# Optimization experiments

Measured on AMD Instinct MI355X. Metric: run time of the kernel, lower is better.

## Reference

```python
import jax, jax.numpy as jnp
import numpy as np

B, C, L, NLAB, EMB, NFREQ, D = 256, 64, 512, 10, 256, 9, 8
FIN, FH, FOUT = 4 * C, C, C
P_TOTAL = FIN * FH + FH + FH * FOUT + FOUT + FIN * FOUT + FOUT


def _leaky(x):
    return jax.nn.leaky_relu(x, 0.2)


def _conv1d(x, w, b=None, pad=0):
    y = jax.lax.conv_general_dilated(x, w, (1,), [(pad, pad)], dimension_numbers=('NCH', 'OIH', 'NCH'))
    return y if b is None else y + b[None, :, None]


def _res1d(x, w0, b0, w1, b1, ws=None, pad=1):
    # GAN-stability style residual block: out = shortcut(x) + 0.1 * conv1(act(conv0(act(x))))
    xs = _conv1d(x, ws) if ws is not None else x
    dx = _conv1d(_leaky(x), w0, b0, pad)
    dx = _conv1d(_leaky(dx), w1, b1, pad)
    return xs + 0.1 * dx


def _pos_enc():
    # sinusoidal positional encoding, 2*NFREQ channels over L positions
    p = np.arange(L, dtype=np.float32)
    f = (np.pi / 2.0 ** np.arange(NFREQ, dtype=np.float32))[:, None]
    pe = np.concatenate([np.sin(f * p), np.cos(f * p)], axis=0)  # [2*NFREQ, L]
    return jnp.asarray(pe)


def _sobel_kernels():
    s = np.array([1.0, 2.0, 1.0], np.float32)
    d = np.array([-1.0, 0.0, 1.0], np.float32)
    kx = np.einsum('i,j,k->ijk', d, s, s)
    ky = np.einsum('i,j,k->ijk', s, d, s)
    kz = np.einsum('i,j,k->ijk', s, s, d)
    return jnp.asarray(np.stack([kx, ky, kz]))  # [3, 3, 3, 3]


def _sin_sobel(x, k):
    # depthwise 3D sobel along each axis, sin of gradients, concat with input -> 4C channels
    outs = [x]
    for i in range(3):
        w = jnp.broadcast_to(k[i][None, None], (C, 1, 3, 3, 3))
        g = jax.lax.conv_general_dilated(x, w, (1, 1, 1), [(1, 1)] * 3,
                                         dimension_numbers=('NCDHW', 'OIDHW', 'NCDHW'),
                                         feature_group_count=C)
        outs.append(jnp.sin(g))
    return jnp.concatenate(outs, axis=1)


def _inst_norm(x):
    m = x.mean(axis=(2, 3, 4), keepdims=True)
    v = x.var(axis=(2, 3, 4), keepdims=True)
    return (x - m) * jax.lax.rsqrt(v + 1e-5)


def _dyna(x, p):
    # hypernet-generated per-sample 1x1x1 residual conv block
    b = x.shape[0]
    xf = x.reshape(b, FIN, D * D * D)
    o = FIN * FH
    wh = p[:, :o].reshape(b, FH, FIN)
    bh = p[:, o:o + FH]; o += FH
    wl = p[:, o:o + FH * FOUT].reshape(b, FOUT, FH); o += FH * FOUT
    bl = p[:, o:o + FOUT]; o += FOUT
    ws = p[:, o:o + FIN * FOUT].reshape(b, FOUT, FIN); o += FIN * FOUT
    bs = p[:, o:o + FOUT]
    xs = jnp.einsum('boi,bis->bos', ws, xf) + bs[:, :, None]
    dx = _leaky(jnp.einsum('bhi,bis->bhs', wh, xf) + bh[:, :, None])
    dx = jnp.einsum('boh,bhs->bos', wl, dx) + bl[:, :, None]
    return (xs + 0.1 * dx).reshape(b, FOUT, D, D, D)


def _forward(codes, y, fc_w, fc_b, in_w0, in_b0, in_w1, in_b1, in_ws, leak, hyper_w, hyper_b,
             out_w0, out_b0, out_w1, out_b1, l1_w0, l1_b0, l1_w1, l1_b1,
             l2_w0, l2_b0, l2_w1, l2_b1, l2_ws):
    b = codes.shape[0]
    yemb = jax.nn.one_hot(y, NLAB, dtype=codes.dtype) @ fc_w.T + fc_b
    yemb = yemb / jnp.maximum(jnp.linalg.norm(yemb, axis=1, keepdims=True), 1e-12)
    pe = jnp.broadcast_to(_pos_enc()[None], (b, 2 * NFREQ, L))
    x = jnp.concatenate([codes, pe], axis=1)  # [B, C+2*NFREQ, L]
    x = _res1d(x, in_w0, in_b0, in_w1, in_b1, ws=in_ws)
    x = x.reshape(b, C, D, D, D)
    leak_c = jnp.clip(leak, 0.001, 1000.0)
    p = yemb @ hyper_w.T + hyper_b  # per-sample dynamic conv params [B, P_TOTAL]
    k = _sobel_kernels()
    for _ in range(8):
        xn = _inst_norm(x)
        xn = _sin_sobel(xn, k)
        xn = _dyna(xn, p)
        x = x + leak_c * xn
    x = x.reshape(b, C, L)
    x = _res1d(x, out_w0, out_b0, out_w1, out_b1)
    code_idx = jnp.argmax(codes, axis=1).reshape(b * L)
    logits = x.transpose(0, 2, 1).reshape(b * L, C)
    logp = jax.nn.log_softmax(logits, axis=-1)
    loss_cent = -jnp.take_along_axis(logp, code_idx[:, None], axis=1).mean()
    lat = _res1d(x, l1_w0, l1_b0, l1_w1, l1_b1, pad=0)
    lat = _res1d(lat, l2_w0, l2_b0, l2_w1, l2_b1, ws=l2_ws, pad=0)
    return lat[:, 0, :], loss_cent


def setup_inputs() -> dict:
    key = jax.random.key(0)
    ks = jax.random.split(key, 16)
    w = lambda k, s: 0.02 * jax.random.normal(k, s, jnp.float32)
    z = lambda s: jnp.zeros(s, jnp.float32)
    CIN = C + 2 * NFREQ  # 82
    return {
        'codes': jax.random.normal(ks[0], (B, C, L), jnp.float32),
        'y': jax.random.randint(ks[1], (B,), 0, NLAB),
        'fc_w': w(ks[2], (EMB, NLAB)), 'fc_b': z((EMB,)),
        'in_w0': w(ks[3], (C, CIN, 3)), 'in_b0': z((C,)),
        'in_w1': w(ks[4], (C, C, 3)), 'in_b1': z((C,)),
        'in_ws': w(ks[5], (C, CIN, 1)),
        'leak': jnp.asarray(0.1, jnp.float32),
        'hyper_w': w(ks[6], (P_TOTAL, EMB)), 'hyper_b': z((P_TOTAL,)),
        'out_w0': w(ks[7], (C, C, 3)), 'out_b0': z((C,)),
        'out_w1': w(ks[8], (C, C, 3)), 'out_b1': z((C,)),
        'l1_w0': w(ks[9], (C, C, 1)), 'l1_b0': z((C,)),
        'l1_w1': w(ks[10], (C, C, 1)), 'l1_b1': z((C,)),
        'l2_w0': w(ks[11], (1, C, 1)), 'l2_b0': z((1,)),
        'l2_w1': w(ks[12], (1, 1, 1)), 'l2_b1': z((1,)),
        'l2_ws': w(ks[13], (1, C, 1)),
    }


def reference(codes, y, fc_w, fc_b, in_w0, in_b0, in_w1, in_b1, in_ws, leak, hyper_w, hyper_b,
              out_w0, out_b0, out_w1, out_b1, l1_w0, l1_b0, l1_w1, l1_b1,
              l2_w0, l2_b0, l2_w1, l2_b1, l2_ws):
    return _forward(codes, y, fc_w, fc_b, in_w0, in_b0, in_w1, in_b1, in_ws, leak, hyper_w, hyper_b,
                    out_w0, out_b0, out_w1, out_b1, l1_w0, l1_b0, l1_w1, l1_b1,
                    l2_w0, l2_b0, l2_w1, l2_b1, l2_ws)
```

## Files before the change

### kernel.cpp

```cpp
#include <hip/hip_runtime.h>

#define B_ 256
#define C_ 64
#define L_ 512
#define CIN_ 82
#define NFREQ_ 9
#define EMB_ 256
#define NLAB_ 10
#define PT_ 37056
#define OFF_BH 16384
#define OFF_WL 16448
#define OFF_BL 20544
#define OFF_WS 20608
#define OFF_BS 36992
#define PI_F 3.14159265358979323846f

typedef short bh8 __attribute__((ext_vector_type(8)));
typedef float f32x4 __attribute__((ext_vector_type(4)));

__device__ inline float lrelu(float v){ return v > 0.f ? v : 0.2f*v; }

__device__ inline unsigned short f2bf(float f){
  unsigned u = __float_as_uint(f);
  u += 0x7FFFu + ((u >> 16) & 1u);
  return (unsigned short)(u >> 16);
}
__device__ inline float bf2f(unsigned short u){
  return __uint_as_float((unsigned)u << 16);
}
__device__ inline unsigned pk2(float a, float b){
  return (unsigned)f2bf(a) | ((unsigned)f2bf(b) << 16);
}
__device__ inline bh8 cvt8(float4 a, float4 b){
  bh8 r;
  r[0]=(short)f2bf(a.x); r[1]=(short)f2bf(a.y); r[2]=(short)f2bf(a.z); r[3]=(short)f2bf(a.w);
  r[4]=(short)f2bf(b.x); r[5]=(short)f2bf(b.y); r[6]=(short)f2bf(b.z); r[7]=(short)f2bf(b.w);
  return r;
}
__device__ inline uint4 pk8(const float* v){
  uint4 o = { pk2(v[0],v[1]), pk2(v[2],v[3]), pk2(v[4],v[5]), pk2(v[6],v[7]) };
  return o;
}
__device__ inline float shf(float v, int a){
  return __uint_as_float((unsigned)__builtin_amdgcn_ds_bpermute(a, (int)__float_as_uint(v)));
}

__global__ __launch_bounds__(256) void k_yemb(const float* __restrict__ fc_w,
    const float* __restrict__ fc_b, const int* __restrict__ y,
    unsigned short* __restrict__ ybf, float* __restrict__ out){
  int b = blockIdx.x, e = threadIdx.x;
  int lab = y[b];
  float v = fc_w[e*NLAB_ + lab] + fc_b[e];
  __shared__ float red[256];
  red[e] = v*v; __syncthreads();
  for (int s = 128; s; s >>= 1){ if (e < s) red[e] += red[e+s]; __syncthreads(); }
  float nrm = fmaxf(sqrtf(red[0]), 1e-12f);
  ybf[(size_t)b*EMB_ + e] = f2bf(v / nrm);
  if (b == 0 && e == 0) out[B_*L_] = 0.f;
}

__global__ __launch_bounds__(256) void k_hyper(const float* __restrict__ hw,
    const float* __restrict__ hb, const unsigned short* __restrict__ ybf,
    unsigned short* __restrict__ p_bf){
  int tid = threadIdx.x;
  int wid = tid >> 6, lane = tid & 63, col = lane & 15, quad = lane >> 4;
  int j = blockIdx.x*64 + wid*16 + col;
  f32x4 acc[16];
  f32x4 z4 = {0.f,0.f,0.f,0.f};
  #pragma unroll
  for (int i = 0; i < 16; i++) acc[i] = z4;
  for (int k0 = 0; k0 < 256; k0 += 32){
    const float* hp = hw + (size_t)j*EMB_ + k0 + quad*8;
    bh8 bf = cvt8(*(const float4*)hp, *(const float4*)(hp+4));
    #pragma unroll
    for (int mt = 0; mt < 16; mt++){
      bh8 af = *(const bh8*)&ybf[(size_t)(mt*16 + col)*EMB_ + k0 + quad*8];
      acc[mt] = __builtin_amdgcn_mfma_f32_16x16x32_bf16(af, bf, acc[mt], 0, 0, 0);
    }
  }
  float hbv = hb[j];
  #pragma unroll
  for (int mt = 0; mt < 16; mt++){
    int b0 = mt*16 + quad*4;
    #pragma unroll
    for (int r = 0; r < 4; r++)
      p_bf[(size_t)(b0 + r)*PT_ + j] = f2bf(acc[mt][r] + hbv);
  }
}

__device__ inline float pe_raw(int fi, int l){
  if (fi < NFREQ_) return __sinf(PI_F / (float)(1 << fi) * (float)l);
  return __cosf(PI_F / (float)(1 << (fi - NFREQ_)) * (float)l);
}

__global__ __launch_bounds__(256) void k_conv_in1(const float* __restrict__ codes,
    const float* __restrict__ w0, const float* __restrict__ b0,
    unsigned short* __restrict__ t1bf){
  int b = blockIdx.x, l0 = blockIdx.y*128, tid = threadIdx.x;
  int wid = tid>>6, lane = tid&63, col = lane&15, quad = lane>>4;
  __shared__ __attribute__((aligned(16))) unsigned short xT[136][96];
  __shared__ __attribute__((aligned(16))) unsigned short wA[3][64][96];
  for (int i = tid; i < 64*96; i += 256){
    int m = i / 96, cin = i % 96;
    if (cin < CIN_){
      const float* s = w0 + (size_t)m*(CIN_*3) + cin*3;
      wA[0][m][cin] = f2bf(s[0]); wA[1][m][cin] = f2bf(s[1]); wA[2][m][cin] = f2bf(s[2]);
    } else { wA[0][m][cin] = 0; wA[1][m][cin] = 0; wA[2][m][cin] = 0; }
  }
  const float* cb = codes + (size_t)b*C_*L_;
  for (int i = tid; i < 96*34; i += 256){
    int c = i / 34, g = i % 34;
    int lg = l0 - 4 + 4*g;
    #pragma unroll
    for (int r2 = 0; r2 < 4; r2++){
      int l = lg + r2;
      float xv = 0.f;
      if (l >= 0 && l < L_){
        if (c < C_) xv = cb[(size_t)c*L_ + l];
        else if (c < CIN_) xv = pe_raw(c - C_, l);
      }
      xT[4*g + r2][c] = f2bf(lrelu(xv));
    }
  }
  __syncthreads();
  f32x4 z4 = {0.f,0.f,0.f,0.f};
  f32x4 acc[8];
  #pragma unroll
  for (int i = 0; i < 8; i++) acc[i] = z4;
  #pragma unroll
  for (int t = 0; t < 3; t++){
    #pragma unroll
    for (int k0 = 0; k0 < 96; k0 += 32){
      bh8 bfr[2];
      #pragma unroll
      for (int nt = 0; nt < 2; nt++)
        bfr[nt] = *(const bh8*)&xT[wid*32 + nt*16 + col + t + 3][k0 + quad*8];
      #pragma unroll
      for (int mt = 0; mt < 4; mt++){
        bh8 af = *(const bh8*)&wA[t][mt*16 + col][k0 + quad*8];
        #pragma unroll
        for (int nt = 0; nt < 2; nt++)
          acc[mt*2+nt] = __builtin_amdgcn_mfma_f32_16x16x32_bf16(af, bfr[nt], acc[mt*2+nt], 0,0,0);
      }
    }
  }
  #pragma unroll
  for (int mt = 0; mt < 4; mt++){
    int f0 = mt*16 + quad*4;
    float q0 = b0[f0], q1 = b0[f0+1], q2 = b0[f0+2], q3 = b0[f0+3];
    #pragma unroll
    for (int nt = 0; nt < 2; nt++){
      int l = l0 + wid*32 + nt*16 + col;
      f32x4 a = acc[mt*2+nt];
      uint2 o = { pk2(lrelu(a[0]+q0), lrelu(a[1]+q1)),
                  pk2(lrelu(a[2]+q2), lrelu(a[3]+q3)) };
      *(uint2*)&t1bf[((size_t)b*L_ + l)*64 + f0] = o;
    }
  }
}

__global__ __launch_bounds__(256) void k_conv_in2(const float* __restrict__ codes,
    const float* __restrict__ wsp, const float* __restrict__ w1, const float* __restrict__ b1,
    const unsigned short* __restrict__ t1bf, float* __restrict__ x){
  int b = blockIdx.x, l0 = blockIdx.y*128, tid = threadIdx.x;
  int wid = tid>>6, lane = tid&63, col = lane&15, quad = lane>>4;
  __shared__ __attribute__((aligned(16))) unsigned short xT[128][96];
  __shared__ __attribute__((aligned(16))) unsigned short wsA[64][96];
  __shared__ __attribute__((aligned(16))) unsigned short w1A[3][64][72];
  for (int i = tid; i < 64*96; i += 256){
    int m = i / 96, cin = i % 96;
    wsA[m][cin] = (cin < CIN_) ? f2bf(wsp[(size_t)m*CIN_ + cin]) : (unsigned short)0;
  }
  for (int i = tid; i < 64*64; i += 256){
    int m = i >> 6, cin = i & 63;
    const float* s = w1 + (size_t)m*192 + cin*3;
    w1A[0][m][cin] = f2bf(s[0]); w1A[1][m][cin] = f2bf(s[1]); w1A[2][m][cin] = f2bf(s[2]);
  }
  const float* cb = codes + (size_t)b*C_*L_;
  for (int i = tid; i < 96*32; i += 256){
    int c = i / 32, g = i % 32;
    int lg = l0 + 4*g;
    #pragma unroll
    for (int r2 = 0; r2 < 4; r2++){
      int l = lg + r2;
      float xv;
      if (c < C_) xv = cb[(size_t)c*L_ + l];
      else if (c < CIN_) xv = pe_raw(c - C_, l);
      else xv = 0.f;
      xT[4*g + r2][c] = f2bf(xv);
    }
  }
  __syncthreads();
  f32x4 z4 = {0.f,0.f,0.f,0.f};
  f32x4 accS[8], accD[8];
  #pragma unroll
  for (int i = 0; i < 8; i++){ accS[i] = z4; accD[i] = z4; }
  #pragma unroll
  for (int k0 = 0; k0 < 96; k0 += 32){
    bh8 bfr[2];
    #pragma unroll
    for (int nt = 0; nt < 2; nt++)
      bfr[nt] = *(const bh8*)&xT[wid*32 + nt*16 + col][k0 + quad*8];
    #pragma unroll
    for (int mt = 0; mt < 4; mt++){
      bh8 af = *(const bh8*)&wsA[mt*16 + col][k0 + quad*8];
      #pragma unroll
      for (int nt = 0; nt < 2; nt++)
        accS[mt*2+nt] = __builtin_amdgcn_mfma_f32_16x16x32_bf16(af, bfr[nt], accS[mt*2+nt], 0,0,0);
    }
  }
  bh8 zz8 = {0,0,0,0,0,0,0,0};
  #pragma unroll
  for (int t = 0; t < 3; t++){
    #pragma unroll
    for (int k0 = 0; k0 < 64; k0 += 32){
      bh8 bfr[2];
      #pragma unroll
      for (int nt = 0; nt < 2; nt++){
        int l = l0 + wid*32 + nt*16 + col + t - 1;
        bfr[nt] = (l >= 0 && l < L_)
          ? *(const bh8*)&t1bf[((size_t)b*L_ + l)*64 + k0 + quad*8] : zz8;
      }
      #pragma unroll
      for (int mt = 0; mt < 4; mt++){
        bh8 af = *(const bh8*)&w1A[t][mt*16 + col][k0 + quad*8];
        #pragma unroll
        for (int nt = 0; nt < 2; nt++)
          accD[mt*2+nt] = __builtin_amdgcn_mfma_f32_16x16x32_bf16(af, bfr[nt], accD[mt*2+nt], 0,0,0);
      }
    }
  }
  #pragma unroll
  for (int mt = 0; mt < 4; mt++){
    int f0 = mt*16 + quad*4;
    float q0 = b1[f0], q1 = b1[f0+1], q2 = b1[f0+2], q3 = b1[f0+3];
    #pragma unroll
    for (int nt = 0; nt < 2; nt++){
      int l = l0 + wid*32 + nt*16 + col;
      f32x4 s = accS[mt*2+nt], d = accD[mt*2+nt];
      size_t base = ((size_t)b*C_ + f0)*L_ + l;
      x[base]        = s[0] + 0.1f*(d[0] + q0);
      x[base + L_]   = s[1] + 0.1f*(d[1] + q1);
      x[base + 2*L_] = s[2] + 0.1f*(d[2] + q2);
      x[base + 3*L_] = s[3] + 0.1f*(d[3] + q3);
    }
  }
}

#define CGS 520
#define GGS 4168
#define TBUF_ 16672
#define SOBEL(CN, TP) { \
      float r[8] = {nv0.x,nv0.y,nv0.z,nv0.w,nv1.x,nv1.y,nv1.z,nv1.w}; \
      if ((CN) < 7){ \
        const float* xp = xb + (size_t)(((CN)+1)*8 + wid)*L_ + lane*8; \
        nv0 = *(const float4*)xp; nv1 = *(const float4*)(xp + 4); \
      } \
      float s1 = 0.f, s2 = 0.f; \
      _Pragma("unroll") \
      for (int i = 0; i < 8; i++){ s1 += r[i]; s2 += r[i]*r[i]; } \
      _Pragma("unroll") \
      for (int m = 32; m; m >>= 1){ s1 += __shfl_xor(s1, m); s2 += __shfl_xor(s2, m); } \
      const float mean = s1 * (1.f/512.f); \
      const float rstd = rsqrtf(s2*(1.f/512.f) - mean*mean + 1e-5f); \
      float xn[8]; \
      _Pragma("unroll") \
      for (int i = 0; i < 8; i++) xn[i] = (r[i]-mean)*rstd; \
      *(uint4*)&(TP)[wid*CGS + lane*8] = pk8(xn); \
      float A[8], Bv[8]; \
      A[0] = 2.f*xn[0]+xn[1]; Bv[0] = xn[1]; \
      _Pragma("unroll") \
      for (int i = 1; i < 7; i++){ A[i] = xn[i-1]+2.f*xn[i]+xn[i+1]; Bv[i] = xn[i+1]-xn[i-1]; } \
      A[7] = xn[6]+2.f*xn[7]; Bv[7] = -xn[6]; \
      float Cv[8], Dv[8], Ev[8]; \
      _Pragma("unroll") \
      for (int i = 0; i < 8; i++){ \
        float am = shf(A[i], lmA)*wm, ap = shf(A[i], lpA)*wp; \
        Cv[i] = am + 2.f*A[i] + ap; \
        Dv[i] = ap - am; \
        float bm = shf(Bv[i], lmA)*wm, bp = shf(Bv[i], lpA)*wp; \
        Ev[i] = bm + 2.f*Bv[i] + bp; \
      } \
      float g0[8], g1[8], g2[8]; \
      _Pragma("unroll") \
      for (int i = 0; i < 8; i++){ \
        g0[i] = __sinf(shf(Cv[i], zpA)*qp - shf(Cv[i], zmA)*qm); \
        g1[i] = __sinf(shf(Dv[i], zmA)*qm + 2.f*Dv[i] + shf(Dv[i], zpA)*qp); \
        g2[i] = __sinf(shf(Ev[i], zmA)*qm + 2.f*Ev[i] + shf(Ev[i], zpA)*qp); \
      } \
      *(uint4*)&(TP)[GGS   + wid*CGS + lane*8] = pk8(g0); \
      *(uint4*)&(TP)[2*GGS + wid*CGS + lane*8] = pk8(g1); \
      *(uint4*)&(TP)[3*GGS + wid*CGS + lane*8] = pk8(g2); \
    }

__global__ __launch_bounds__(512, 1) void k_loop(float* __restrict__ x,
    const unsigned short* __restrict__ p_bf, const float* __restrict__ leak){
  const int b = blockIdx.x, tid = threadIdx.x;
  const int wid = tid >> 6, lane = tid & 63, col = lane & 15, quad = lane >> 4;
  const int yy = lane & 7, zz = lane >> 3;
  const unsigned short* pb = p_bf + (size_t)b*PT_;
  float* xb = x + (size_t)b*C_*L_;

  __shared__ __attribute__((aligned(16))) unsigned short SMEM[36864];
  unsigned short* Tb = SMEM;
  unsigned short (*h_t)[72] = (unsigned short (*)[72])SMEM;

  const int lmA = ((yy > 0) ? lane-1 : lane)*4;  const float wm = (yy > 0) ? 1.f : 0.f;
  const int lpA = ((yy < 7) ? lane+1 : lane)*4;  const float wp = (yy < 7) ? 1.f : 0.f;
  const int zmA = ((zz > 0) ? lane-8 : lane)*4;  const float qm = (zz > 0) ? 1.f : 0.f;
  const int zpA = ((zz < 7) ? lane+8 : lane)*4;  const float qp = (zz < 7) ? 1.f : 0.f;

  const float lk = fminf(fmaxf(leak[0], 0.001f), 1000.f);
  const f32x4 z4 = {0.f,0.f,0.f,0.f};

  for (int it = 0; it < 8; ++it){
    f32x4 acc1[32];
    #pragma unroll
    for (int i = 0; i < 32; i++) acc1[i] = z4;

    float4 nv0, nv1;
    { const float* xp = xb + (size_t)wid*L_ + lane*8;
      nv0 = *(const float4*)xp; nv1 = *(const float4*)(xp + 4); }
    SOBEL(0, Tb)
    __syncthreads();

    #pragma unroll 2
    for (int cc = 0; cc < 8; ++cc){
      unsigned short* Tc = Tb + (cc&1)*TBUF_;
      unsigned short* Tn = Tb + ((cc+1)&1)*TBUF_;
      if (cc < 7) SOBEL(cc+1, Tn)
      { bh8 bfr[4];
        #pragma unroll
        for (int nt = 0; nt < 4; nt++){
          const int n = wid*64 + nt*16 + col;
          bh8 fv;
          #pragma unroll
          for (int j = 0; j < 8; j++) fv[j] = (short)Tc[quad*GGS + j*CGS + n];
          bfr[nt] = fv;
        }
        const int kof = quad*64 + cc*8;
        #pragma unroll
        for (int mt = 0; mt < 8; mt++){
          bh8 af = (mt < 4)
            ? *(const bh8*)&pb[(size_t)(mt*16+col)*256 + kof]
            : *(const bh8*)&pb[OFF_WS + (size_t)((mt-4)*16+col)*256 + kof];
          #pragma unroll
          for (int nt = 0; nt < 4; nt++)
            acc1[mt*4+nt] = __builtin_amdgcn_mfma_f32_16x16x32_bf16(af, bfr[nt], acc1[mt*4+nt], 0,0,0);
        }
      }
      __syncthreads();
    }

    #pragma unroll
    for (int mt = 0; mt < 4; mt++){
      const int f0 = mt*16 + quad*4;
      const float bh0 = bf2f(pb[OFF_BH+f0]),   bh1 = bf2f(pb[OFF_BH+f0+1]);
      const float bh2 = bf2f(pb[OFF_BH+f0+2]), bh3 = bf2f(pb[OFF_BH+f0+3]);
      #pragma unroll
      for (int nt = 0; nt < 4; nt++){
        const int n = wid*64 + nt*16 + col;
        f32x4 a = acc1[mt*4+nt];
        uint2 o = { pk2(lrelu(a[0]+bh0), lrelu(a[1]+bh1)),
                    pk2(lrelu(a[2]+bh2), lrelu(a[3]+bh3)) };
        *(uint2*)&h_t[n][f0] = o;
      }
    }
    f32x4 acc2[16];
    #pragma unroll
    for (int i = 0; i < 16; i++) acc2[i] = z4;
    #pragma unroll
    for (int k0 = 0; k0 < 64; k0 += 32){
      bh8 hb[4];
      #pragma unroll
      for (int nt = 0; nt < 4; nt++)
        hb[nt] = *(const bh8*)&h_t[wid*64 + nt*16 + col][k0 + quad*8];
      #pragma unroll
      for (int mt = 0; mt < 4; mt++){
        bh8 al = *(const bh8*)&pb[OFF_WL + (size_t)(mt*16 + col)*64 + k0 + quad*8];
        #pragma unroll
        for (int nt = 0; nt < 4; nt++)
          acc2[mt*4+nt] = __builtin_amdgcn_mfma_f32_16x16x32_bf16(al, hb[nt], acc2[mt*4+nt], 0,0,0);
      }
    }
    #pragma unroll
    for (int mt = 0; mt < 4; mt++){
      const int f0 = mt*16 + quad*4;
      const float bs0 = bf2f(pb[OFF_BS+f0]),   bs1 = bf2f(pb[OFF_BS+f0+1]);
      const float bs2 = bf2f(pb[OFF_BS+f0+2]), bs3 = bf2f(pb[OFF_BS+f0+3]);
      const float bl0 = bf2f(pb[OFF_BL+f0]),   bl1 = bf2f(pb[OFF_BL+f0+1]);
      const float bl2 = bf2f(pb[OFF_BL+f0+2]), bl3 = bf2f(pb[OFF_BL+f0+3]);
      #pragma unroll
      for (int nt = 0; nt < 4; nt++){
        const int n = wid*64 + nt*16 + col;
        f32x4 xs = acc1[(mt+4)*4+nt], dx = acc2[mt*4+nt];
        size_t xi = (size_t)f0*L_ + n;
        xb[xi]        += lk*(xs[0] + bs0 + 0.1f*(dx[0] + bl0));
        xb[xi + L_]   += lk*(xs[1] + bs1 + 0.1f*(dx[1] + bl1));
        xb[xi + 2*L_] += lk*(xs[2] + bs2 + 0.1f*(dx[2] + bl2));
        xb[xi + 3*L_] += lk*(xs[3] + bs3 + 0.1f*(dx[3] + bl3));
      }
    }
    __threadfence_block();
    __syncthreads();
  }
}

__global__ __launch_bounds__(256) void k_conv_out1(const float* __restrict__ x,
    const float* __restrict__ w, const float* __restrict__ bias,
    unsigned short* __restrict__ t1bf){
  int b = blockIdx.x, l0 = blockIdx.y*128, tid = threadIdx.x;
  int wid = tid>>6, lane = tid&63, col = lane&15, quad = lane>>4;
  __shared__ __attribute__((aligned(16))) unsigned short xT[136][72];
  __shared__ __attribute__((aligned(16))) unsigned short wA[3][64][72];
  for (int i = tid; i < 64*64; i += 256){
    int m = i >> 6, cin = i & 63;
    const float* s = w + (size_t)m*192 + cin*3;
    wA[0][m][cin] = f2bf(s[0]); wA[1][m][cin] = f2bf(s[1]); wA[2][m][cin] = f2bf(s[2]);
  }
  const float* xb = x + (size_t)b*C_*L_;
  for (int i = tid; i < 64*34; i += 256){
    int c = i / 34, g = i % 34;
    int lg = l0 - 4 + 4*g;
    if (lg >= 0 && lg + 3 < L_){
      float4 f = *(const float4*)&xb[(size_t)c*L_ + lg];
      xT[4*g  ][c] = f2bf(lrelu(f.x));
      xT[4*g+1][c] = f2bf(lrelu(f.y));
      xT[4*g+2][c] = f2bf(lrelu(f.z));
      xT[4*g+3][c] = f2bf(lrelu(f.w));
    } else {
      #pragma unroll
      for (int r2 = 0; r2 < 4; r2++){
        int l = lg + r2;
        float v = (l >= 0 && l < L_) ? xb[(size_t)c*L_ + l] : 0.f;
        xT[4*g + r2][c] = f2bf(lrelu(v));
      }
    }
  }
  __syncthreads();
  f32x4 z4 = {0.f,0.f,0.f,0.f};
  f32x4 acc[8];
  #pragma unroll
  for (int i = 0; i < 8; i++) acc[i] = z4;
  #pragma unroll
  for (int t = 0; t < 3; t++){
    #pragma unroll
    for (int k0 = 0; k0 < 64; k0 += 32){
      bh8 bfr[2];
      #pragma unroll
      for (int nt = 0; nt < 2; nt++)
        bfr[nt] = *(const bh8*)&xT[wid*32 + nt*16 + col + t + 3][k0 + quad*8];
      #pragma unroll
      for (int mt = 0; mt < 4; mt++){
        bh8 af = *(const bh8*)&wA[t][mt*16 + col][k0 + quad*8];
        #pragma unroll
        for (int nt = 0; nt < 2; nt++)
          acc[mt*2+nt] = __builtin_amdgcn_mfma_f32_16x16x32_bf16(af, bfr[nt], acc[mt*2+nt], 0,0,0);
      }
    }
  }
  #pragma unroll
  for (int mt = 0; mt < 4; mt++){
    int f0 = mt*16 + quad*4;
    float q0 = bias[f0], q1 = bias[f0+1], q2 = bias[f0+2], q3 = bias[f0+3];
    #pragma unroll
    for (int nt = 0; nt < 2; nt++){
      int l = l0 + wid*32 + nt*16 + col;
      f32x4 a = acc[mt*2+nt];
      uint2 o = { pk2(lrelu(a[0]+q0), lrelu(a[1]+q1)),
                  pk2(lrelu(a[2]+q2), lrelu(a[3]+q3)) };
      *(uint2*)&t1bf[((size_t)b*L_ + l)*64 + f0] = o;
    }
  }
}

__global__ __launch_bounds__(256) void k_conv_out2(float* __restrict__ x,
    const unsigned short* __restrict__ t1bf, const float* __restrict__ w,
    const float* __restrict__ bias){
  int b = blockIdx.x, l0 = blockIdx.y*256, tid = threadIdx.x;
  int wid = tid>>6, lane = tid&63, col = lane&15, quad = lane>>4;
  __shared__ __attribute__((aligned(16))) unsigned short wA[3][64][72];
  for (int i = tid; i < 64*64; i += 256){
    int m = i >> 6, cin = i & 63;
    const float* s = w + (size_t)m*192 + cin*3;
    wA[0][m][cin] = f2bf(s[0]); wA[1][m][cin] = f2bf(s[1]); wA[2][m][cin] = f2bf(s[2]);
  }
  __syncthreads();
  f32x4 z4 = {0.f,0.f,0.f,0.f};
  f32x4 acc[16];
  #pragma unroll
  for (int i = 0; i < 16; i++) acc[i] = z4;
  bh8 zz8 = {0,0,0,0,0,0,0,0};
  #pragma unroll
  for (int t = 0; t < 3; t++){
    #pragma unroll
    for (int k0 = 0; k0 < 64; k0 += 32){
      bh8 bfr[4];
      #pragma unroll
      for (int nt = 0; nt < 4; nt++){
        int l = l0 + wid*64 + nt*16 + col + t - 1;
        bfr[nt] = (l >= 0 && l < L_)
          ? *(const bh8*)&t1bf[((size_t)b*L_ + l)*64 + k0 + quad*8] : zz8;
      }
      #pragma unroll
      for (int mt = 0; mt < 4; mt++){
        bh8 af = *(const bh8*)&wA[t][mt*16 + col][k0 + quad*8];
        #pragma unroll
        for (int nt = 0; nt < 4; nt++)
          acc[mt*4+nt] = __builtin_amdgcn_mfma_f32_16x16x32_bf16(af, bfr[nt], acc[mt*4+nt], 0,0,0);
      }
    }
  }
  #pragma unroll
  for (int mt = 0; mt < 4; mt++){
    int f0 = mt*16 + quad*4;
    float q0 = bias[f0], q1 = bias[f0+1], q2 = bias[f0+2], q3 = bias[f0+3];
    #pragma unroll
    for (int nt = 0; nt < 4; nt++){
      int l = l0 + wid*64 + nt*16 + col;
      f32x4 a = acc[mt*4+nt];
      size_t base = ((size_t)b*C_ + f0)*L_ + l;
      x[base]        += 0.1f*(a[0] + q0);
      x[base + L_]   += 0.1f*(a[1] + q1);
      x[base + 2*L_] += 0.1f*(a[2] + q2);
      x[base + 3*L_] += 0.1f*(a[3] + q3);
    }
  }
}

__global__ __launch_bounds__(256) void k_loss(const float* __restrict__ x,
    const float* __restrict__ codes, float* __restrict__ out){
  int b = blockIdx.x;
  int l = blockIdx.y*256 + threadIdx.x;
  const float* xb = x + (size_t)b*C_*L_ + l;
  const float* cb = codes + (size_t)b*C_*L_ + l;
  float m = -1e30f, cm = -1e30f;
  int ci = 0;
  for (int c = 0; c < C_; c++){
    float xv = xb[(size_t)c*L_];
    m = fmaxf(m, xv);
    float cv = cb[(size_t)c*L_];
    if (cv > cm){ cm = cv; ci = c; }
  }
  float s = 0.f, vi = 0.f;
  for (int c = 0; c < C_; c++){
    float xv = xb[(size_t)c*L_];
    s += expf(xv - m);
    if (c == ci) vi = xv;
  }
  float lp = vi - m - logf(s);
  __shared__ float red[256];
  red[threadIdx.x] = -lp; __syncthreads();
  for (int sft = 128; sft; sft >>= 1){
    if (threadIdx.x < sft) red[threadIdx.x] += red[threadIdx.x + sft];
    __syncthreads();
  }
  if (threadIdx.x == 0) atomicAdd(out + B_*L_, red[0] * (1.0f/131072.0f));
}

__global__ __launch_bounds__(256) void k_lat(const float* __restrict__ x,
    const float* __restrict__ w10, const float* __restrict__ b10,
    const float* __restrict__ w11, const float* __restrict__ b11,
    const float* __restrict__ w20, const float* __restrict__ b20,
    const float* __restrict__ w21, const float* __restrict__ b21,
    const float* __restrict__ ws2, float* __restrict__ out){
  int b = blockIdx.x, l0 = blockIdx.y*256;
  int tid = threadIdx.x;
  int wid = tid >> 6, lane = tid & 63, col = lane & 15, quad = lane >> 4;
  __shared__ __attribute__((aligned(16))) unsigned short wA[2][64][72];
  __shared__ __attribute__((aligned(16))) unsigned short Bt[256][72];

  for (int i = tid; i < 1024; i += 256){
    int arr = i >> 9, rem = i & 511, row = rem >> 3, seg = rem & 7;
    const float* src = (arr ? w11 : w10) + (size_t)row*C_ + seg*8;
    *(bh8*)&wA[arr][row][seg*8] = cvt8(*(const float4*)src, *(const float4*)(src+4));
  }
  for (int i = tid; i < 4096; i += 256){
    int c = i >> 6, seg = i & 63;
    float4 v = *(const float4*)&x[((size_t)b*C_ + c)*L_ + l0 + seg*4];
    Bt[seg*4+0][c] = f2bf(lrelu(v.x));
    Bt[seg*4+1][c] = f2bf(lrelu(v.y));
    Bt[seg*4+2][c] = f2bf(lrelu(v.z));
    Bt[seg*4+3][c] = f2bf(lrelu(v.w));
  }
  __syncthreads();
  f32x4 z4 = {0.f,0.f,0.f,0.f};
  f32x4 acc1[16];
  #pragma unroll
  for (int i = 0; i < 16; i++) acc1[i] = z4;
  #pragma unroll
  for (int k0 = 0; k0 < 64; k0 += 32){
    bh8 bfr[4];
    #pragma unroll
    for (int nt = 0; nt < 4; nt++)
      bfr[nt] = *(const bh8*)&Bt[wid*64 + nt*16 + col][k0 + quad*8];
    #pragma unroll
    for (int mt = 0; mt < 4; mt++){
      bh8 af = *(const bh8*)&wA[0][mt*16 + col][k0 + quad*8];
      #pragma unroll
      for (int nt = 0; nt < 4; nt++)
        acc1[mt*4+nt] = __builtin_amdgcn_mfma_f32_16x16x32_bf16(af, bfr[nt], acc1[mt*4+nt], 0, 0, 0);
    }
  }
  #pragma unroll
  for (int mt = 0; mt < 4; mt++){
    int f0 = mt*16 + quad*4;
    f32x4 bv = *(const f32x4*)&b10[f0];
    #pragma unroll
    for (int nt = 0; nt < 4; nt++){
      int n = wid*64 + nt*16 + col;
      f32x4 a = acc1[mt*4+nt];
      uint2 o = { pk2(lrelu(a[0]+bv[0]), lrelu(a[1]+bv[1])),
                  pk2(lrelu(a[2]+bv[2]), lrelu(a[3]+bv[3])) };
      *(uint2*)&Bt[n][f0] = o;
    }
  }
  f32x4 acc2[16];
  #pragma unroll
  for (int i = 0; i < 16; i++) acc2[i] = z4;
  #pragma unroll
  for (int k0 = 0; k0 < 64; k0 += 32){
    bh8 bfr[4];
    #pragma unroll
    for (int nt = 0; nt < 4; nt++)
      bfr[nt] = *(const bh8*)&Bt[wid*64 + nt*16 + col][k0 + quad*8];
    #pragma unroll
    for (int mt = 0; mt < 4; mt++){
      bh8 af = *(const bh8*)&wA[1][mt*16 + col][k0 + quad*8];
      #pragma unroll
      for (int nt = 0; nt < 4; nt++)
        acc2[mt*4+nt] = __builtin_amdgcn_mfma_f32_16x16x32_bf16(af, bfr[nt], acc2[mt*4+nt], 0, 0, 0);
    }
  }
  float psA[4] = {0.f,0.f,0.f,0.f}, psB[4] = {0.f,0.f,0.f,0.f};
  #pragma unroll
  for (int mt = 0; mt < 4; mt++){
    int f0 = mt*16 + quad*4;
    f32x4 b11v = *(const f32x4*)&b11[f0];
    f32x4 wsv  = *(const f32x4*)&ws2[f0];
    f32x4 w20v = *(const f32x4*)&w20[f0];
    #pragma unroll
    for (int nt = 0; nt < 4; nt++){
      int lg = l0 + wid*64 + nt*16 + col;
      size_t base = ((size_t)b*C_ + f0)*L_ + lg;
      f32x4 a = acc2[mt*4+nt];
      #pragma unroll
      for (int r = 0; r < 4; r++){
        float xv = x[base + (size_t)r*L_];
        float lat = xv + 0.1f*(a[r] + b11v[r]);
        psA[nt] += wsv[r]*lat;
        psB[nt] += w20v[r]*lrelu(lat);
      }
    }
  }
  #pragma unroll
  for (int nt = 0; nt < 4; nt++){
    psA[nt] += __shfl_xor(psA[nt], 16); psA[nt] += __shfl_xor(psA[nt], 32);
    psB[nt] += __shfl_xor(psB[nt], 16); psB[nt] += __shfl_xor(psB[nt], 32);
  }
  if (quad == 0){
    float b20s = b20[0], w21s = w21[0], b21s = b21[0];
    #pragma unroll
    for (int nt = 0; nt < 4; nt++){
      float dx2 = w21s*lrelu(psB[nt] + b20s) + b21s;
      out[(size_t)b*L_ + l0 + wid*64 + nt*16 + col] = psA[nt] + 0.1f*dx2;
    }
  }
}

extern "C" void kernel_launch(void* const* d_in, const int* in_sizes, int n_in,
                              void* d_out, int out_size, void* d_ws, size_t ws_size,
                              hipStream_t stream) {
  (void)in_sizes; (void)n_in; (void)out_size; (void)ws_size;
  const float* codes   = (const float*)d_in[0];
  const int*   y       = (const int*)  d_in[1];
  const float* fc_w    = (const float*)d_in[2];
  const float* fc_b    = (const float*)d_in[3];
  const float* in_w0   = (const float*)d_in[4];
  const float* in_b0   = (const float*)d_in[5];
  const float* in_w1   = (const float*)d_in[6];
  const float* in_b1   = (const float*)d_in[7];
  const float* in_wsp  = (const float*)d_in[8];
  const float* leak    = (const float*)d_in[9];
  const float* hyper_w = (const float*)d_in[10];
  const float* hyper_b = (const float*)d_in[11];
  const float* out_w0  = (const float*)d_in[12];
  const float* out_b0  = (const float*)d_in[13];
  const float* out_w1  = (const float*)d_in[14];
  const float* out_b1  = (const float*)d_in[15];
  const float* l1_w0   = (const float*)d_in[16];
  const float* l1_b0   = (const float*)d_in[17];
  const float* l1_w1   = (const float*)d_in[18];
  const float* l1_b1   = (const float*)d_in[19];
  const float* l2_w0   = (const float*)d_in[20];
  const float* l2_b0   = (const float*)d_in[21];
  const float* l2_w1   = (const float*)d_in[22];
  const float* l2_b1   = (const float*)d_in[23];
  const float* l2_ws   = (const float*)d_in[24];
  float* out = (float*)d_out;

  char* ws = (char*)d_ws;
  unsigned short* p_bf = (unsigned short*)(ws);
  unsigned short* ybf  = (unsigned short*)(ws + 18972672);
  float* x             = (float*)(ws + 19103744);
  unsigned short* t1bf = (unsigned short*)(ws + 52658176);

  k_yemb<<<B_, 256, 0, stream>>>(fc_w, fc_b, y, ybf, out);
  k_hyper<<<PT_/64, 256, 0, stream>>>(hyper_w, hyper_b, ybf, p_bf);
  k_conv_in1<<<dim3(B_, 4), 256, 0, stream>>>(codes, in_w0, in_b0, t1bf);
  k_conv_in2<<<dim3(B_, 4), 256, 0, stream>>>(codes, in_wsp, in_w1, in_b1, t1bf, x);
  k_loop<<<B_, 512, 0, stream>>>(x, p_bf, leak);
  k_conv_out1<<<dim3(B_, 4), 256, 0, stream>>>(x, out_w0, out_b0, t1bf);
  k_conv_out2<<<dim3(B_, 2), 256, 0, stream>>>(x, t1bf, out_w1, out_b1);
  k_loss<<<dim3(B_, 2), 256, 0, stream>>>(x, codes, out);
  k_lat<<<dim3(B_, 2), 256, 0, stream>>>(x, l1_w0, l1_b0, l1_w1, l1_b1,
                                         l2_w0, l2_b0, l2_w1, l2_b1, l2_ws, out);
}
```

Before: 855.8 us.

## Defer residual update into LDS bf16 buffer and apply during next Sobel load

Instead of a strided global read-modify-write of x after each loop iteration, the residual increment is written as bf16 into a new LDS buffer and added to x when the next iteration's Sobel stage loads those rows, writing x back coalesced. The last iteration still updates global x directly. This removes one global read pass and scattered stores per iteration, at the cost of much more LDS and rounding the increment to bf16.

```diff
diff --git a/kernel.cpp b/kernel.cpp
--- a/kernel.cpp
+++ b/kernel.cpp
@@ -250,8 +250,19 @@
 #define CGS 520
 #define GGS 4168
 #define TBUF_ 16672
+#define UST 520
 #define SOBEL(CN, TP) { \
       float r[8] = {nv0.x,nv0.y,nv0.z,nv0.w,nv1.x,nv1.y,nv1.z,nv1.w}; \
+      if (aplu){ \
+        const uint4 uv = *(const uint4*)&Ub[(size_t)((CN)*8 + wid)*UST + lane*8]; \
+        r[0] += bf2f((unsigned short)(uv.x & 0xffffu)); r[1] += bf2f((unsigned short)(uv.x >> 16)); \
+        r[2] += bf2f((unsigned short)(uv.y & 0xffffu)); r[3] += bf2f((unsigned short)(uv.y >> 16)); \
+        r[4] += bf2f((unsigned short)(uv.z & 0xffffu)); r[5] += bf2f((unsigned short)(uv.z >> 16)); \
+        r[6] += bf2f((unsigned short)(uv.w & 0xffffu)); r[7] += bf2f((unsigned short)(uv.w >> 16)); \
+        float* xw = xb + (size_t)((CN)*8 + wid)*L_ + lane*8; \
+        float4 w0 = {r[0],r[1],r[2],r[3]}, w1 = {r[4],r[5],r[6],r[7]}; \
+        *(float4*)xw = w0; *(float4*)(xw + 4) = w1; \
+      } \
       if ((CN) < 7){ \
         const float* xp = xb + (size_t)(((CN)+1)*8 + wid)*L_ + lane*8; \
         nv0 = *(const float4*)xp; nv1 = *(const float4*)(xp + 4); \
@@ -301,9 +312,10 @@
   const unsigned short* pb = p_bf + (size_t)b*PT_;
   float* xb = x + (size_t)b*C_*L_;
 
-  __shared__ __attribute__((aligned(16))) unsigned short SMEM[36864];
+  __shared__ __attribute__((aligned(16))) unsigned short SMEM[36864 + 64*UST];
   unsigned short* Tb = SMEM;
   unsigned short (*h_t)[72] = (unsigned short (*)[72])SMEM;
+  unsigned short* Ub = SMEM + 36864;
 
   const int lmA = ((yy > 0) ? lane-1 : lane)*4;  const float wm = (yy > 0) ? 1.f : 0.f;
   const int lpA = ((yy < 7) ? lane+1 : lane)*4;  const float wp = (yy < 7) ? 1.f : 0.f;
@@ -314,6 +326,7 @@
   const f32x4 z4 = {0.f,0.f,0.f,0.f};
 
   for (int it = 0; it < 8; ++it){
+    const bool aplu = (it > 0);
     f32x4 acc1[32];
     #pragma unroll
     for (int i = 0; i < 32; i++) acc1[i] = z4;
@@ -383,22 +396,45 @@
           acc2[mt*4+nt] = __builtin_amdgcn_mfma_f32_16x16x32_bf16(al, hb[nt], acc2[mt*4+nt], 0,0,0);
       }
     }
-    #pragma unroll
-    for (int mt = 0; mt < 4; mt++){
-      const int f0 = mt*16 + quad*4;
-      const float bs0 = bf2f(pb[OFF_BS+f0]),   bs1 = bf2f(pb[OFF_BS+f0+1]);
-      const float bs2 = bf2f(pb[OFF_BS+f0+2]), bs3 = bf2f(pb[OFF_BS+f0+3]);
-      const float bl0 = bf2f(pb[OFF_BL+f0]),   bl1 = bf2f(pb[OFF_BL+f0+1]);
-      const float bl2 = bf2f(pb[OFF_BL+f0+2]), bl3 = bf2f(pb[OFF_BL+f0+3]);
-      #pragma unroll
-      for (int nt = 0; nt < 4; nt++){
-        const int n = wid*64 + nt*16 + col;
-        f32x4 xs = acc1[(mt+4)*4+nt], dx = acc2[mt*4+nt];
-        size_t xi = (size_t)f0*L_ + n;
-        xb[xi]        += lk*(xs[0] + bs0 + 0.1f*(dx[0] + bl0));
-        xb[xi + L_]   += lk*(xs[1] + bs1 + 0.1f*(dx[1] + bl1));
-        xb[xi + 2*L_] += lk*(xs[2] + bs2 + 0.1f*(dx[2] + bl2));
-        xb[xi + 3*L_] += lk*(xs[3] + bs3 + 0.1f*(dx[3] + bl3));
+
+    if (it < 7){
+      #pragma unroll
+      for (int mt = 0; mt < 4; mt++){
+        const int f0 = mt*16 + quad*4;
+        const float bs0 = bf2f(pb[OFF_BS+f0]),   bs1 = bf2f(pb[OFF_BS+f0+1]);
+        const float bs2 = bf2f(pb[OFF_BS+f0+2]), bs3 = bf2f(pb[OFF_BS+f0+3]);
+        const float bl0 = bf2f(pb[OFF_BL+f0]),   bl1 = bf2f(pb[OFF_BL+f0+1]);
+        const float bl2 = bf2f(pb[OFF_BL+f0+2]), bl3 = bf2f(pb[OFF_BL+f0+3]);
+        #pragma unroll
+        for (int nt = 0; nt < 4; nt++){
+          const int n = wid*64 + nt*16 + col;
+          f32x4 xs = acc1[(mt+4)*4+nt], dx = acc2[mt*4+nt];
+          Ub[(size_t)(f0+0)*UST + n] = f2bf(lk*(xs[0] + bs0 + 0.1f*(dx[0] + bl0)));
+          Ub[(size_t)(f0+1)*UST + n] = f2bf(lk*(xs[1] + bs1 + 0.1f*(dx[1] + bl1)));
+          Ub[(size_t)(f0+2)*UST + n] = f2bf(lk*(xs[2] + bs2 + 0.1f*(dx[2] + bl2)));
+          Ub[(size_t)(f0+3)*UST + n] = f2bf(lk*(xs[3] + bs3 + 0.1f*(dx[3] + bl3)));
+        }
+      }
+    } else {
+      __threadfence_block();
+      __syncthreads();
+      #pragma unroll
+      for (int mt = 0; mt < 4; mt++){
+        const int f0 = mt*16 + quad*4;
+        const float bs0 = bf2f(pb[OFF_BS+f0]),   bs1 = bf2f(pb[OFF_BS+f0+1]);
+        const float bs2 = bf2f(pb[OFF_BS+f0+2]), bs3 = bf2f(pb[OFF_BS+f0+3]);
+        const float bl0 = bf2f(pb[OFF_BL+f0]),   bl1 = bf2f(pb[OFF_BL+f0+1]);
+        const float bl2 = bf2f(pb[OFF_BL+f0+2]), bl3 = bf2f(pb[OFF_BL+f0+3]);
+        #pragma unroll
+        for (int nt = 0; nt < 4; nt++){
+          const int n = wid*64 + nt*16 + col;
+          f32x4 xs = acc1[(mt+4)*4+nt], dx = acc2[mt*4+nt];
+          size_t xi = (size_t)f0*L_ + n;
+          xb[xi]        += lk*(xs[0] + bs0 + 0.1f*(dx[0] + bl0));
+          xb[xi + L_]   += lk*(xs[1] + bs1 + 0.1f*(dx[1] + bl1));
+          xb[xi + 2*L_] += lk*(xs[2] + bs2 + 0.1f*(dx[2] + bl2));
+          xb[xi + 3*L_] += lk*(xs[3] + bs3 + 0.1f*(dx[3] + bl3));
+        }
       }
     }
     __threadfence_block();
```

Measured after the change: 836.8 us. 2.2% less time.

## Keep per-sample activations resident in LDS across loop iterations

Applied to the files above, without the earlier changes.

Loads the whole per-sample activation tensor (64x512 fp32, 128KB) into shared memory once, runs all eight hypernet residual iterations against it, and writes it back to global memory only at the end. This removes the repeated global reads and read-modify-writes of x each iteration. To fit the LDS budget, the Sobel feature buffer drops from double-buffered to single-buffered, with an extra barrier per channel group, and its padding is replaced by XOR swizzles. The second GEMM stage is split into two wave groups that take turns using a reduced scratch slab, which serializes half the waves. The A-fragment loads are also split into two batches of four to lower register pressure.

```diff
diff --git a/kernel.cpp b/kernel.cpp
--- a/kernel.cpp
+++ b/kernel.cpp
@@ -247,15 +247,10 @@
   }
 }
 
-#define CGS 520
-#define GGS 4168
-#define TBUF_ 16672
-#define SOBEL(CN, TP) { \
-      float r[8] = {nv0.x,nv0.y,nv0.z,nv0.w,nv1.x,nv1.y,nv1.z,nv1.w}; \
-      if ((CN) < 7){ \
-        const float* xp = xb + (size_t)(((CN)+1)*8 + wid)*L_ + lane*8; \
-        nv0 = *(const float4*)xp; nv1 = *(const float4*)(xp + 4); \
-      } \
+#define SOBEL(CN) { \
+      const float* xr_ = &xl[(size_t)((CN)*8 + wid)*L_ + lane*8]; \
+      float4 v0_ = *(const float4*)xr_, v1_ = *(const float4*)(xr_ + 4); \
+      float r[8] = {v0_.x,v0_.y,v0_.z,v0_.w,v1_.x,v1_.y,v1_.z,v1_.w}; \
       float s1 = 0.f, s2 = 0.f; \
       _Pragma("unroll") \
       for (int i = 0; i < 8; i++){ s1 += r[i]; s2 += r[i]*r[i]; } \
@@ -266,7 +261,7 @@
       float xn[8]; \
       _Pragma("unroll") \
       for (int i = 0; i < 8; i++) xn[i] = (r[i]-mean)*rstd; \
-      *(uint4*)&(TP)[wid*CGS + lane*8] = pk8(xn); \
+      *(uint4*)&Tb[wid*512 + lane*8] = pk8(xn); \
       float A[8], Bv[8]; \
       A[0] = 2.f*xn[0]+xn[1]; Bv[0] = xn[1]; \
       _Pragma("unroll") \
@@ -288,9 +283,9 @@
         g1[i] = __sinf(shf(Dv[i], zmA)*qm + 2.f*Dv[i] + shf(Dv[i], zpA)*qp); \
         g2[i] = __sinf(shf(Ev[i], zmA)*qm + 2.f*Ev[i] + shf(Ev[i], zpA)*qp); \
       } \
-      *(uint4*)&(TP)[GGS   + wid*CGS + lane*8] = pk8(g0); \
-      *(uint4*)&(TP)[2*GGS + wid*CGS + lane*8] = pk8(g1); \
-      *(uint4*)&(TP)[3*GGS + wid*CGS + lane*8] = pk8(g2); \
+      *(uint4*)&Tb[4096  + wid*512 + ((lane*8) ^ 16)] = pk8(g0); \
+      *(uint4*)&Tb[8192  + wid*512 + ((lane*8) ^ 32)] = pk8(g1); \
+      *(uint4*)&Tb[12288 + wid*512 + ((lane*8) ^ 48)] = pk8(g2); \
     }
 
 __global__ __launch_bounds__(512, 1) void k_loop(float* __restrict__ x,
@@ -299,11 +294,11 @@
   const int wid = tid >> 6, lane = tid & 63, col = lane & 15, quad = lane >> 4;
   const int yy = lane & 7, zz = lane >> 3;
   const unsigned short* pb = p_bf + (size_t)b*PT_;
-  float* xb = x + (size_t)b*C_*L_;
-
-  __shared__ __attribute__((aligned(16))) unsigned short SMEM[36864];
-  unsigned short* Tb = SMEM;
-  unsigned short (*h_t)[72] = (unsigned short (*)[72])SMEM;
+  float* xg = x + (size_t)b*C_*L_;
+
+  __shared__ __attribute__((aligned(16))) unsigned short SMEM[81920];
+  float* xl = (float*)SMEM;
+  unsigned short* Tb = SMEM + 65536;
 
   const int lmA = ((yy > 0) ? lane-1 : lane)*4;  const float wm = (yy > 0) ? 1.f : 0.f;
   const int lpA = ((yy < 7) ? lane+1 : lane)*4;  const float wp = (yy < 7) ? 1.f : 0.f;
@@ -313,96 +308,125 @@
   const float lk = fminf(fmaxf(leak[0], 0.001f), 1000.f);
   const f32x4 z4 = {0.f,0.f,0.f,0.f};
 
+  #pragma unroll
+  for (int g = 0; g < 8; g++){
+    const float* s = xg + (size_t)(g*8 + wid)*L_ + lane*8;
+    float4 a = *(const float4*)s, c2 = *(const float4*)(s + 4);
+    float* d = &xl[(size_t)(g*8 + wid)*L_ + lane*8];
+    *(float4*)d = a; *(float4*)(d + 4) = c2;
+  }
+  __syncthreads();
+
   for (int it = 0; it < 8; ++it){
     f32x4 acc1[32];
     #pragma unroll
     for (int i = 0; i < 32; i++) acc1[i] = z4;
 
-    float4 nv0, nv1;
-    { const float* xp = xb + (size_t)wid*L_ + lane*8;
-      nv0 = *(const float4*)xp; nv1 = *(const float4*)(xp + 4); }
-    SOBEL(0, Tb)
-    __syncthreads();
-
     #pragma unroll 2
     for (int cc = 0; cc < 8; ++cc){
-      unsigned short* Tc = Tb + (cc&1)*TBUF_;
-      unsigned short* Tn = Tb + ((cc+1)&1)*TBUF_;
-      if (cc < 7) SOBEL(cc+1, Tn)
+      SOBEL(cc)
+      __syncthreads();
       { bh8 bfr[4];
         #pragma unroll
         for (int nt = 0; nt < 4; nt++){
           const int n = wid*64 + nt*16 + col;
           bh8 fv;
           #pragma unroll
-          for (int j = 0; j < 8; j++) fv[j] = (short)Tc[quad*GGS + j*CGS + n];
+          for (int j = 0; j < 8; j++)
+            fv[j] = (short)Tb[quad*4096 + j*512 + (n ^ (quad<<4))];
           bfr[nt] = fv;
         }
         const int kof = quad*64 + cc*8;
-        #pragma unroll
-        for (int mt = 0; mt < 8; mt++){
-          bh8 af = (mt < 4)
-            ? *(const bh8*)&pb[(size_t)(mt*16+col)*256 + kof]
-            : *(const bh8*)&pb[OFF_WS + (size_t)((mt-4)*16+col)*256 + kof];
+        bh8 ah[4];
+        #pragma unroll
+        for (int mt = 0; mt < 4; mt++)
+          ah[mt] = *(const bh8*)&pb[(size_t)(mt*16+col)*256 + kof];
+        #pragma unroll
+        for (int mt = 0; mt < 4; mt++){
           #pragma unroll
           for (int nt = 0; nt < 4; nt++)
-            acc1[mt*4+nt] = __builtin_amdgcn_mfma_f32_16x16x32_bf16(af, bfr[nt], acc1[mt*4+nt], 0,0,0);
+            acc1[mt*4+nt] = __builtin_amdgcn_mfma_f32_16x16x32_bf16(ah[mt], bfr[nt], acc1[mt*4+nt], 0,0,0);
         }
+        #pragma unroll
+        for (int mt = 0; mt < 4; mt++)
+          ah[mt] = *(const bh8*)&pb[OFF_WS + (size_t)(mt*16+col)*256 + kof];
+        #pragma unroll
+        for (int mt = 0; mt < 4; mt++){
+          #pragma unroll
+          for (int nt = 0; nt < 4; nt++)
+            acc1[(mt+4)*4+nt] = __builtin_amdgcn_mfma_f32_16x16x32_bf16(ah[mt], bfr[nt], acc1[(mt+4)*4+nt], 0,0,0);
+        }
       }
       __syncthreads();
     }
 
-    #pragma unroll
-    for (int mt = 0; mt < 4; mt++){
-      const int f0 = mt*16 + quad*4;
-      const float bh0 = bf2f(pb[OFF_BH+f0]),   bh1 = bf2f(pb[OFF_BH+f0+1]);
-      const float bh2 = bf2f(pb[OFF_BH+f0+2]), bh3 = bf2f(pb[OFF_BH+f0+3]);
-      #pragma unroll
-      for (int nt = 0; nt < 4; nt++){
-        const int n = wid*64 + nt*16 + col;
-        f32x4 a = acc1[mt*4+nt];
-        uint2 o = { pk2(lrelu(a[0]+bh0), lrelu(a[1]+bh1)),
-                    pk2(lrelu(a[2]+bh2), lrelu(a[3]+bh3)) };
-        *(uint2*)&h_t[n][f0] = o;
-      }
-    }
-    f32x4 acc2[16];
-    #pragma unroll
-    for (int i = 0; i < 16; i++) acc2[i] = z4;
-    #pragma unroll
-    for (int k0 = 0; k0 < 64; k0 += 32){
-      bh8 hb[4];
-      #pragma unroll
-      for (int nt = 0; nt < 4; nt++)
-        hb[nt] = *(const bh8*)&h_t[wid*64 + nt*16 + col][k0 + quad*8];
-      #pragma unroll
-      for (int mt = 0; mt < 4; mt++){
-        bh8 al = *(const bh8*)&pb[OFF_WL + (size_t)(mt*16 + col)*64 + k0 + quad*8];
-        #pragma unroll
-        for (int nt = 0; nt < 4; nt++)
-          acc2[mt*4+nt] = __builtin_amdgcn_mfma_f32_16x16x32_bf16(al, hb[nt], acc2[mt*4+nt], 0,0,0);
-      }
-    }
-    #pragma unroll
-    for (int mt = 0; mt < 4; mt++){
-      const int f0 = mt*16 + quad*4;
-      const float bs0 = bf2f(pb[OFF_BS+f0]),   bs1 = bf2f(pb[OFF_BS+f0+1]);
-      const float bs2 = bf2f(pb[OFF_BS+f0+2]), bs3 = bf2f(pb[OFF_BS+f0+3]);
-      const float bl0 = bf2f(pb[OFF_BL+f0]),   bl1 = bf2f(pb[OFF_BL+f0+1]);
-      const float bl2 = bf2f(pb[OFF_BL+f0+2]), bl3 = bf2f(pb[OFF_BL+f0+3]);
-      #pragma unroll
-      for (int nt = 0; nt < 4; nt++){
-        const int n = wid*64 + nt*16 + col;
-        f32x4 xs = acc1[(mt+4)*4+nt], dx = acc2[mt*4+nt];
-        size_t xi = (size_t)f0*L_ + n;
-        xb[xi]        += lk*(xs[0] + bs0 + 0.1f*(dx[0] + bl0));
-        xb[xi + L_]   += lk*(xs[1] + bs1 + 0.1f*(dx[1] + bl1));
-        xb[xi + 2*L_] += lk*(xs[2] + bs2 + 0.1f*(dx[2] + bl2));
-        xb[xi + 3*L_] += lk*(xs[3] + bs3 + 0.1f*(dx[3] + bl3));
-      }
-    }
-    __threadfence_block();
-    __syncthreads();
+    #pragma unroll 1
+    for (int sg = 0; sg < 2; ++sg){
+      if ((wid >> 2) == sg){
+        unsigned short* slab = Tb + (wid & 3)*4096;
+        #pragma unroll
+        for (int mt = 0; mt < 4; mt++){
+          const int f0 = mt*16 + quad*4;
+          const float bh0 = bf2f(pb[OFF_BH+f0]),   bh1 = bf2f(pb[OFF_BH+f0+1]);
+          const float bh2 = bf2f(pb[OFF_BH+f0+2]), bh3 = bf2f(pb[OFF_BH+f0+3]);
+          #pragma unroll
+          for (int nt = 0; nt < 4; nt++){
+            const int nl = nt*16 + col;
+            const int kx = f0 ^ ((col & 7) << 3);
+            f32x4 a = acc1[mt*4+nt];
+            uint2 o = { pk2(lrelu(a[0]+bh0), lrelu(a[1]+bh1)),
+                        pk2(lrelu(a[2]+bh2), lrelu(a[3]+bh3)) };
+            *(uint2*)&slab[nl*64 + kx] = o;
+          }
+        }
+        f32x4 acc2[16];
+        #pragma unroll
+        for (int i = 0; i < 16; i++) acc2[i] = z4;
+        #pragma unroll
+        for (int k0 = 0; k0 < 64; k0 += 32){
+          bh8 hb[4];
+          #pragma unroll
+          for (int nt = 0; nt < 4; nt++){
+            const int nl = nt*16 + col;
+            const int kx = (k0 + quad*8) ^ ((col & 7) << 3);
+            hb[nt] = *(const bh8*)&slab[nl*64 + kx];
+          }
+          #pragma unroll
+          for (int mt = 0; mt < 4; mt++){
+            bh8 al = *(const bh8*)&pb[OFF_WL + (size_t)(mt*16 + col)*64 + k0 + quad*8];
+            #pragma unroll
+            for (int nt = 0; nt < 4; nt++)
+              acc2[mt*4+nt] = __builtin_amdgcn_mfma_f32_16x16x32_bf16(al, hb[nt], acc2[mt*4+nt], 0,0,0);
+          }
+        }
+        #pragma unroll
+        for (int mt = 0; mt < 4; mt++){
+          const int f0 = mt*16 + quad*4;
+          const float bs0 = bf2f(pb[OFF_BS+f0]),   bs1 = bf2f(pb[OFF_BS+f0+1]);
+          const float bs2 = bf2f(pb[OFF_BS+f0+2]), bs3 = bf2f(pb[OFF_BS+f0+3]);
+          const float bl0 = bf2f(pb[OFF_BL+f0]),   bl1 = bf2f(pb[OFF_BL+f0+1]);
+          const float bl2 = bf2f(pb[OFF_BL+f0+2]), bl3 = bf2f(pb[OFF_BL+f0+3]);
+          #pragma unroll
+          for (int nt = 0; nt < 4; nt++){
+            const int n = wid*64 + nt*16 + col;
+            f32x4 xs = acc1[(mt+4)*4+nt], dx = acc2[mt*4+nt];
+            xl[(size_t)(f0+0)*L_ + n] += lk*(xs[0] + bs0 + 0.1f*(dx[0] + bl0));
+            xl[(size_t)(f0+1)*L_ + n] += lk*(xs[1] + bs1 + 0.1f*(dx[1] + bl1));
+            xl[(size_t)(f0+2)*L_ + n] += lk*(xs[2] + bs2 + 0.1f*(dx[2] + bl2));
+            xl[(size_t)(f0+3)*L_ + n] += lk*(xs[3] + bs3 + 0.1f*(dx[3] + bl3));
+          }
+        }
+      }
+      __syncthreads();
+    }
+  }
+
+  #pragma unroll
+  for (int g = 0; g < 8; g++){
+    const float* s = &xl[(size_t)(g*8 + wid)*L_ + lane*8];
+    float4 a = *(const float4*)s, c2 = *(const float4*)(s + 4);
+    float* d = xg + (size_t)(g*8 + wid)*L_ + lane*8;
+    *(float4*)d = a; *(float4*)(d + 4) = c2;
   }
 }
 
```

New measurement: 856.5 us. Within noise of the previous version (+0.1%).
